# Kernel tuning notes

Measured on AMD Instinct MI355X. Metric: run time of the kernel, lower is better.

The kernel has to match this reference:

```python
import jax, jax.numpy as jnp
import numpy as np

# Multi-scale AvgPool3d pyramid (stride 1, zero padding, count_include_pad=True as in torch)
KERNELS = [(1, 1, 1), (1, 5, 5), (3, 13, 13), (5, 23, 23), (7, 31, 31), (9, 41, 41)]
WEIGHTS = [w / 100.0 for w in [20, 20, 20, 20, 20, 20, 10, 10]]
EPS = 1e-7  # BatchDiceLoss epsilon


def avgpool3d(x, k):
    # x: [B, C, D, H, W]; separable sum-pool per axis then divide by full kernel size
    # (equivalent to torch AvgPool3d with count_include_pad=True, stride 1, pad=(k-1)//2)
    y = x
    for axis, ks in zip((2, 3, 4), k):
        if ks > 1:
            window = [1] * 5
            window[axis] = ks
            pad = [(0, 0)] * 5
            pad[axis] = (ks // 2, ks // 2)
            y = jax.lax.reduce_window(y, 0.0, jax.lax.add, tuple(window), (1,) * 5, tuple(pad))
    return y / float(np.prod(k))


def batch_dice(pred, target):
    # BatchDiceLoss([1.0]): single label channel 0, flattened over the whole batch
    p = pred[:, 0].reshape(-1)
    t = target[:, 0].reshape(-1)
    inter = jnp.sum(p * t)
    return 1.0 - (2.0 * inter) / (jnp.sum(p) + jnp.sum(t) + EPS)


def multi_scale_dc(pred, target):
    loss = 0.0
    for k in KERNELS:
        pp = avgpool3d(avgpool3d(pred, k), k)   # pool applied twice per scale
        tt = avgpool3d(avgpool3d(target, k), k)
        loss = loss + batch_dice(pp, tt)
    return loss / len(KERNELS)


def setup_inputs() -> dict:
    key = jax.random.key(0)
    ks = jax.random.split(key, 14)
    vol = (4, 1, 28, 160, 160)
    u = lambda k: jax.random.uniform(k, vol, dtype=jnp.float32)
    return {
        "pr_core_c": u(ks[0]),
        "pr_core_p": u(ks[1]),
        "gt_core": u(ks[2]),
        "pr_lesion_c": u(ks[3]),
        "pr_lesion_p": u(ks[4]),
        "gt_lesion": u(ks[5]),
        "pr_penu_c": u(ks[6]),
        "pr_penu_p": u(ks[7]),
        "gt_penu": u(ks[8]),
        "output": jax.random.uniform(ks[9], (4, 6, 28, 160, 160), dtype=jnp.float32),
        "off_core_c": jax.random.normal(ks[10], (4, 3), dtype=jnp.float32),
        "off_penu_p": jax.random.normal(ks[11], (4, 3), dtype=jnp.float32),
        "off_target_c": jax.random.normal(ks[12], (4, 3), dtype=jnp.float32),
        "off_target_p": jax.random.normal(ks[13], (4, 3), dtype=jnp.float32),
    }


def reference(pr_core_c, pr_core_p, gt_core, pr_lesion_c, pr_lesion_p, gt_lesion,
              pr_penu_c, pr_penu_p, gt_penu, output,
              off_core_c, off_penu_p, off_target_c, off_target_p):
    loss = WEIGHTS[0] * multi_scale_dc(pr_core_c, gt_core)
    loss += WEIGHTS[1] * multi_scale_dc(pr_core_p, gt_core)
    loss += WEIGHTS[2] * multi_scale_dc(pr_lesion_c, gt_lesion)
    loss += WEIGHTS[3] * multi_scale_dc(pr_lesion_p, gt_lesion)
    loss += WEIGHTS[4] * multi_scale_dc(pr_penu_c, gt_penu)
    loss += WEIGHTS[5] * multi_scale_dc(pr_penu_p, gt_penu)
    # temporal monotonicity penalty: mean(|diff| - diff) per consecutive time pair
    diff = output[:, 1:] - output[:, :-1]           # [B, T-1, D, H, W]
    loss += WEIGHTS[6] * jnp.sum(jnp.mean(jnp.abs(diff) - diff, axis=(0, 2, 3, 4)))
    loss += WEIGHTS[7] * jnp.mean(jnp.abs(off_core_c - off_target_c))
    loss += WEIGHTS[7] * jnp.mean(jnp.abs(off_penu_p - off_target_p))
    return loss
```

## Files before the change

kernel.cpp:

```cpp
#include <hip/hip_runtime.h>
#include <hip/hip_fp16.h>


#define DIMB 4
#define DIMD 28
#define DIMH 160
#define DIMW 160
#define HW   (DIMH * DIMW)
#define DHW  (DIMD * HW)
#define VOL_N (DIMB * DHW)
#define PGRID 640
#define NSLOTS 91
#define DICE_EPS 1e-7

__device__ __forceinline__ float u2f(int pos, int k, int L) {
    if (k == 1) return 1.f;
    int r = k >> 1;
    float s = 0.f;
    for (int j = max(pos - r, 0); j <= min(pos + r, L - 1); ++j)
        s += (float)(min(j + r, L - 1) - max(j - r, 0) + 1);
    return s / (float)(k * k);
}

__device__ __forceinline__ float wave_sum(float v) {
#pragma unroll
    for (int o = 1; o < 64; o <<= 1) v += __shfl_xor(v, o, 64);
    return v;
}

template<int K>
__device__ __forceinline__ void box4_col(float (&x)[28]) {
    constexpr int R = K / 2;
    constexpr float INVK = 1.f / (float)K;
#pragma unroll
    for (int p = 0; p < 4; ++p) {
        float y[28];
        float s = 0.f;
#pragma unroll
        for (int j = 0; j <= R; ++j) s += x[j];
        y[0] = s;
#pragma unroll
        for (int i = 1; i < 28; ++i) {
            if (i + R < 28) s += x[i + R];
            if (i - R - 1 >= 0) s -= x[i - R - 1];
            y[i] = s;
        }
#pragma unroll
        for (int i = 0; i < 28; ++i) x[i] = y[i] * INVK;
    }
}

template<int K>
__device__ __forceinline__ void hbody(const float* __restrict__ base,
                                      __half* __restrict__ ob, int t)
{
    constexpr int R = K / 2;
    constexpr float INVK = 1.f / (float)K;
    int l = t & 63, v = t >> 6;
    int c = l >> 4;
    int wl = v * 16 + (l & 15);
    int h0 = c * 40;
    float ox[40];
#pragma unroll
    for (int i = 0; i < 40; ++i) ox[i] = base[(h0 + i) * DIMW + wl];
#pragma unroll
    for (int pass = 0; pass < 4; ++pass) {
        float lo[R], hi[R];
#pragma unroll
        for (int i = 0; i < R; ++i) {
            float a = __shfl(ox[40 - R + i], l - 16, 64);
            lo[i] = (c == 0) ? 0.f : a;
            float b = __shfl(ox[i], l + 16, 64);
            hi[i] = (c == 3) ? 0.f : b;
        }
#define HWIN(j) ((j) < R ? lo[(j)] : ((j) < R + 40 ? ox[(j) - R] : hi[(j) - R - 40]))
        float out[40];
        float s = 0.f;
#pragma unroll
        for (int j = 0; j <= 2 * R; ++j) s += HWIN(j);
        out[0] = s * INVK;
#pragma unroll
        for (int i = 1; i < 40; ++i) {
            s += HWIN(i + 2 * R) - HWIN(i - 1);
            out[i] = s * INVK;
        }
#undef HWIN
#pragma unroll
        for (int i = 0; i < 40; ++i) ox[i] = out[i];
    }
#pragma unroll
    for (int i = 0; i < 40; ++i) ob[(h0 + i) * DIMW + wl] = __float2half(ox[i]);
}

__device__ __forceinline__ void hpool_run(const float* in, __half* ob5, int sc,
                                          int bd, int wt, int t)
{
    const float* base = in + (size_t)bd * HW + wt * 32;
    __half* ob = ob5 + (size_t)sc * VOL_N + (size_t)bd * HW + wt * 32;
    switch (sc) {
        case 0: hbody<5>(base, ob, t); break;
        case 1: hbody<13>(base, ob, t); break;
        case 2: hbody<23>(base, ob, t); break;
        case 3: hbody<31>(base, ob, t); break;
        default: hbody<41>(base, ob, t); break;
    }
}

__global__ __launch_bounds__(256) void hpool_mono(const float* __restrict__ g0,
    const float* __restrict__ g1, const float* __restrict__ g2,
    const float* __restrict__ o6, __half* __restrict__ bufs,
    double* __restrict__ partials)
{
    __shared__ float redSm[4];
    int bx = blockIdx.x;
    if (bx < 4200) {
        int u = bx * 2 + (threadIdx.x >> 7);
        int tt = threadIdx.x & 127;
        int gg = u / 2800, r0 = u - gg * 2800;
        int sc = r0 / 560, r = r0 - sc * 560;
        const float* in = (gg == 0) ? g0 : (gg == 1) ? g1 : g2;
        hpool_run(in, bufs + (size_t)gg * 5 * VOL_N, sc, r / 5, r % 5, tt);
    } else {
        int mb = bx - 4200;
        const int N4 = VOL_N / 4, PB = N4 / DIMB;
        float acc = 0.f;
        const float4* p = (const float4*)o6;
        for (int i = mb * 256 + threadIdx.x; i < N4; i += PGRID * 256) {
            int b = i / PB, r4 = i - b * PB;
            size_t a = (size_t)(b * 6) * PB + r4;
            float4 prev = p[a];
#pragma unroll
            for (int cc = 1; cc < 6; ++cc) {
                float4 cur = p[a + (size_t)cc * PB];
                acc += fmaxf(prev.x - cur.x, 0.f) + fmaxf(prev.y - cur.y, 0.f)
                     + fmaxf(prev.z - cur.z, 0.f) + fmaxf(prev.w - cur.w, 0.f);
                prev = cur;
            }
        }
        float rv = wave_sum(acc * 2.f);
        int lane = threadIdx.x & 63, wid = threadIdx.x >> 6;
        if (lane == 0) redSm[wid] = rv;
        __syncthreads();
        if (threadIdx.x == 0)
            partials[(size_t)90 * PGRID + mb] =
                (double)redSm[0] + redSm[1] + redSm[2] + redSm[3];
    }
}

template<int K, int KD>
__device__ __forceinline__ void scale_work(const uint2 (&rg)[5],
    float (*S)[164], int t, int l, int c, int rr, bool act,
    const float* __restrict__ pc, const float* __restrict__ pp,
    size_t base0, float& aic, float& aip)
{
    constexpr int R = K / 2;
    constexpr float INVK = 1.f / (float)K;
    float ox[20];
#pragma unroll
    for (int i = 0; i < 20; ++i) ox[i] = 0.f;
    if (act) {
#pragma unroll
        for (int q = 0; q < 5; ++q) {
            __half2 a = *reinterpret_cast<const __half2*>(&rg[q].x);
            __half2 b = *reinterpret_cast<const __half2*>(&rg[q].y);
            float2 fa = __half22float2(a), fb = __half22float2(b);
            ox[4*q+0] = fa.x; ox[4*q+1] = fa.y;
            ox[4*q+2] = fb.x; ox[4*q+3] = fb.y;
        }
    }
#pragma unroll
    for (int pass = 0; pass < 4; ++pass) {
        float lo[R], hi[R];
#pragma unroll
        for (int i = 0; i < R; ++i) {
            float a = __shfl(ox[20 - R + i], l - 1, 64);
            lo[i] = (c == 0) ? 0.f : a;
            float b = __shfl(ox[i], l + 1, 64);
            hi[i] = (c == 7) ? 0.f : b;
        }
#define WWIN(j) ((j) < R ? lo[(j)] : ((j) < R + 20 ? ox[(j) - R] : hi[(j) - R - 20]))
        float out[20];
        float s = 0.f;
#pragma unroll
        for (int j = 0; j <= 2 * R; ++j) s += WWIN(j);
        out[0] = s * INVK;
#pragma unroll
        for (int i = 1; i < 20; ++i) {
            s += WWIN(i + 2 * R) - WWIN(i - 1);
            out[i] = s * INVK;
        }
#undef WWIN
#pragma unroll
        for (int i = 0; i < 20; ++i) ox[i] = out[i];
    }
    if (act) {
#pragma unroll
        for (int i = 0; i < 20; ++i) S[rr][c * 20 + i] = ox[i];
    }
    __syncthreads();
    if constexpr (KD > 1) {
        if (t < DIMW) {
            float col[28];
#pragma unroll
            for (int j = 0; j < 28; ++j) col[j] = S[j][t];
            box4_col<KD>(col);
#pragma unroll
            for (int j = 0; j < 28; ++j) S[j][t] = col[j];
        }
        __syncthreads();
    }
    for (int e4 = t; e4 < 280; e4 += 256) {
        int dd = e4 / 40, w4 = e4 - dd * 40;
        size_t gb = base0 + (size_t)dd * HW + 4 * w4;
        float4 vc = *(const float4*)(pc + gb);
        float4 vp = *(const float4*)(pp + gb);
        float t0 = S[dd][4*w4], t1 = S[dd][4*w4+1];
        float t2 = S[dd][4*w4+2], t3 = S[dd][4*w4+3];
        aic += vc.x*t0 + vc.y*t1 + vc.z*t2 + vc.w*t3;
        aip += vp.x*t0 + vp.y*t1 + vp.z*t2 + vp.w*t3;
    }
    __syncthreads();
}

__global__ __launch_bounds__(256) void wd5(const __half* __restrict__ bufs,
    const float* __restrict__ pc0, const float* __restrict__ pp0,
    const float* __restrict__ pc1, const float* __restrict__ pp1,
    const float* __restrict__ pc2, const float* __restrict__ pp2,
    const float* __restrict__ tr0, const float* __restrict__ tr1,
    const float* __restrict__ tr2, double* __restrict__ partials)
{
    __shared__ float S[DIMD][164];
    __shared__ float cD[6][DIMD], cW[6][DIMW];
    __shared__ float redS[4][22];
    int bx = blockIdx.x;
    int grp = bx / 1920, r = bx - grp * 1920;
    int g = r / PGRID, bh = r - g * PGRID;
    int b = bh / DIMH, h = bh - b * DIMH;
    size_t base0 = (size_t)b * DHW + (size_t)h * DIMW;
    const float* pc = (g == 0) ? pc0 : (g == 1) ? pc1 : pc2;
    const float* pp = (g == 0) ? pp0 : (g == 1) ? pp1 : pp2;
    int t = threadIdx.x;
    int l = t & 63;
    int rr = (t >> 6) * 7 + (l >> 3), c = l & 7;
    bool act = l < 56;
    const __half* tb = bufs + (size_t)g * 5 * VOL_N + base0
                     + (size_t)rr * HW + c * 20;
    int wid = t >> 6;

    if (grp == 0) {
        const float* tr = (g == 0) ? tr0 : (g == 1) ? tr1 : tr2;
        const int KDa[6] = {1, 1, 3, 5, 7, 9};
        const int KHa[6] = {1, 5, 13, 23, 31, 41};
        for (int e = t; e < 6 * DIMD; e += 256) {
            int s = e / DIMD, q = e - s * DIMD;
            cD[s][q] = u2f(q, KDa[s], DIMD);
        }
        for (int e = t; e < 6 * DIMW; e += 256) {
            int s = e / DIMW, q = e - s * DIMW;
            cW[s][q] = u2f(q, KHa[s], DIMW);
        }
        __syncthreads();
        uint2 rA[5];
        if (act) {
            const __half* hp = tb + (size_t)4 * VOL_N;
#pragma unroll
            for (int q = 0; q < 5; ++q) rA[q] = *(const uint2*)(hp + 4 * q);
        }
        float vals[22];
#pragma unroll
        for (int i = 0; i < 22; ++i) vals[i] = 0.f;
        for (int e4 = t; e4 < 280; e4 += 256) {
            int dd = e4 / 40, w4 = e4 - dd * 40;
            size_t gb = base0 + (size_t)dd * HW + 4 * w4;
            float4 vt = *(const float4*)(tr + gb);
            float4 vc = *(const float4*)(pc + gb);
            float4 vp = *(const float4*)(pp + gb);
            vals[0] += vc.x*vt.x + vc.y*vt.y + vc.z*vt.z + vc.w*vt.w;
            vals[1] += vp.x*vt.x + vp.y*vt.y + vp.z*vt.z + vp.w*vt.w;
#pragma unroll
            for (int s = 0; s < 6; ++s) {
                float cdh = cD[s][dd];
                float w0 = cdh * cW[s][4*w4+0], w1 = cdh * cW[s][4*w4+1];
                float w2 = cdh * cW[s][4*w4+2], w3 = cdh * cW[s][4*w4+3];
                vals[2+s]  += w0*vc.x + w1*vc.y + w2*vc.z + w3*vc.w;
                vals[8+s]  += w0*vp.x + w1*vp.y + w2*vp.z + w3*vp.w;
                vals[14+s] += w0*vt.x + w1*vt.y + w2*vt.z + w3*vt.w;
            }
        }
        scale_work<41, 9>(rA, S, t, l, c, rr, act, pc, pp, base0,
                          vals[20], vals[21]);
#pragma unroll
        for (int i = 0; i < 22; ++i) {
            float rv = wave_sum(vals[i]);
            if (l == 0) redS[wid][i] = rv;
        }
        __syncthreads();
        if (t < 22) {
            double rv = (double)redS[0][t] + redS[1][t] + redS[2][t] + redS[3][t];
            int slot; double fac = 1.0;
            if (t == 0) slot = (2 * g) * 6;
            else if (t == 1) slot = (2 * g + 1) * 6;
            else if (t < 20) {
                int i = t - 2, vv = i / 6, s = i % 6;
                fac = (double)cW[s][h];
                slot = (vv == 0) ? 36 + (2 * g) * 6 + s
                     : (vv == 1) ? 36 + (2 * g + 1) * 6 + s
                                 : 72 + g * 6 + s;
            }
            else if (t == 20) slot = (2 * g) * 6 + 5;
            else slot = (2 * g + 1) * 6 + 5;
            partials[(size_t)slot * PGRID + bh] = rv * fac;
        }
    } else {
        uint2 rA[5], rB[5];
        int scA = (grp == 1) ? 0 : 1;
        int scB = (grp == 1) ? 3 : 2;
        if (act) {
            const __half* ha = tb + (size_t)scA * VOL_N;
            const __half* hb = tb + (size_t)scB * VOL_N;
#pragma unroll
            for (int q = 0; q < 5; ++q) rA[q] = *(const uint2*)(ha + 4 * q);
#pragma unroll
            for (int q = 0; q < 5; ++q) rB[q] = *(const uint2*)(hb + 4 * q);
        }
        float vals[4] = {0.f, 0.f, 0.f, 0.f};
        if (grp == 1) {
            scale_work<5, 1>(rA, S, t, l, c, rr, act, pc, pp, base0, vals[0], vals[1]);
            scale_work<31, 7>(rB, S, t, l, c, rr, act, pc, pp, base0, vals[2], vals[3]);
        } else {
            scale_work<13, 3>(rA, S, t, l, c, rr, act, pc, pp, base0, vals[0], vals[1]);
            scale_work<23, 5>(rB, S, t, l, c, rr, act, pc, pp, base0, vals[2], vals[3]);
        }
#pragma unroll
        for (int i = 0; i < 4; ++i) {
            float rv = wave_sum(vals[i]);
            if (l == 0) redS[wid][i] = rv;
        }
        __syncthreads();
        if (t < 4) {
            double rv = (double)redS[0][t] + redS[1][t] + redS[2][t] + redS[3][t];
            int sd = (t < 2) ? ((grp == 1) ? 1 : 2) : ((grp == 1) ? 4 : 3);
            int slot = (2 * g + (t & 1)) * 6 + sd;
            partials[(size_t)slot * PGRID + bh] = rv;
        }
    }
}

__global__ __launch_bounds__(64) void fin_pre(const double* __restrict__ partials,
                                              double* __restrict__ ssum)
{
    int slot = blockIdx.x, t = threadIdx.x;
    double a = 0.0;
    for (int i = t; i < PGRID; i += 64) a += partials[(size_t)slot * PGRID + i];
#pragma unroll
    for (int o = 1; o < 64; o <<= 1) a += __shfl_xor(a, o, 64);
    if (t == 0) ssum[slot] = a;
}

__global__ void finalize(const double* __restrict__ ssum,
                         const float* __restrict__ off_a,
                         const float* __restrict__ off_b,
                         const float* __restrict__ off_ta,
                         const float* __restrict__ off_tb,
                         float* __restrict__ out)
{
    if (threadIdx.x == 0) {
        double loss = 0.0;
        for (int pair = 0; pair < 6; ++pair) {
            for (int s = 0; s < 6; ++s) {
                double inter = ssum[pair * 6 + s];
                double sp = ssum[36 + pair * 6 + s];
                double st = ssum[72 + (pair / 2) * 6 + s];
                loss += 0.2 * (1.0 - 2.0 * inter / (sp + st + DICE_EPS)) / 6.0;
            }
        }
        loss += 0.1 * (ssum[90] / (double)VOL_N);
        double oa = 0.0, ob = 0.0;
        for (int i = 0; i < 12; ++i) {
            oa += fabs((double)off_a[i] - (double)off_ta[i]);
            ob += fabs((double)off_b[i] - (double)off_tb[i]);
        }
        loss += 0.1 * (oa / 12.0) + 0.1 * (ob / 12.0);
        out[0] = (float)loss;
    }
}

extern "C" void kernel_launch(void* const* d_in, const int* in_sizes, int n_in,
                              void* d_out, int out_size, void* d_ws, size_t ws_size,
                              hipStream_t stream)
{
    double* partials = (double*)d_ws;
    double* ssum = partials + (size_t)NSLOTS * PGRID;
    __half* bufs = (__half*)((char*)d_ws + 512 * 1024);

    const float* pred[6] = {(const float*)d_in[0], (const float*)d_in[1],
                            (const float*)d_in[3], (const float*)d_in[4],
                            (const float*)d_in[6], (const float*)d_in[7]};
    const float* gt[3] = {(const float*)d_in[2], (const float*)d_in[5],
                          (const float*)d_in[8]};

    hpool_mono<<<4840, 256, 0, stream>>>(gt[0], gt[1], gt[2],
                                         (const float*)d_in[9], bufs, partials);
    wd5<<<5760, 256, 0, stream>>>(bufs, pred[0], pred[1], pred[2], pred[3],
                                  pred[4], pred[5], gt[0], gt[1], gt[2], partials);
    fin_pre<<<NSLOTS, 64, 0, stream>>>(partials, ssum);
    finalize<<<1, 64, 0, stream>>>(ssum,
                                   (const float*)d_in[10], (const float*)d_in[11],
                                   (const float*)d_in[12], (const float*)d_in[13],
                                   (float*)d_out);
}
```

Before: 139.8 us.

## Store H-pooled targets as 8-bit and split per-scale dot blocks

The H-direction pooled target intermediates are now written as unsigned 8-bit values scaled by 255 instead of fp16, and the 1/255 is folded into the first W pass when they are read back. One block now loads each raw target tile once and produces all five scales. The W/D pooling kernel is reorganised into one block per scale and row, with the D-column box filter fused straight into the dot product with predictions. The unpooled sums move into a separate flat-grid section. This cuts intermediate memory traffic and repeated loads, at the cost of quantisation error and the assumption that pooled targets lie in [0,1].

```diff
diff --git a/kernel.cpp b/kernel.cpp
--- a/kernel.cpp
+++ b/kernel.cpp
@@ -1,5 +1,4 @@
 #include <hip/hip_runtime.h>
-#include <hip/hip_fp16.h>
 
 
 #define DIMB 4
@@ -51,18 +50,15 @@
 }
 
 template<int K>
-__device__ __forceinline__ void hbody(const float* __restrict__ base,
-                                      __half* __restrict__ ob, int t)
+__device__ __forceinline__ void hstore(const float (&raw)[40],
+                                       unsigned char* __restrict__ ob,
+                                       int l, int c, int wl, int h0)
 {
     constexpr int R = K / 2;
     constexpr float INVK = 1.f / (float)K;
-    int l = t & 63, v = t >> 6;
-    int c = l >> 4;
-    int wl = v * 16 + (l & 15);
-    int h0 = c * 40;
     float ox[40];
 #pragma unroll
-    for (int i = 0; i < 40; ++i) ox[i] = base[(h0 + i) * DIMW + wl];
+    for (int i = 0; i < 40; ++i) ox[i] = raw[i];
 #pragma unroll
     for (int pass = 0; pass < 4; ++pass) {
         float lo[R], hi[R];
@@ -89,39 +85,37 @@
         for (int i = 0; i < 40; ++i) ox[i] = out[i];
     }
 #pragma unroll
-    for (int i = 0; i < 40; ++i) ob[(h0 + i) * DIMW + wl] = __float2half(ox[i]);
-}
-
-__device__ __forceinline__ void hpool_run(const float* in, __half* ob5, int sc,
-                                          int bd, int wt, int t)
-{
-    const float* base = in + (size_t)bd * HW + wt * 32;
-    __half* ob = ob5 + (size_t)sc * VOL_N + (size_t)bd * HW + wt * 32;
-    switch (sc) {
-        case 0: hbody<5>(base, ob, t); break;
-        case 1: hbody<13>(base, ob, t); break;
-        case 2: hbody<23>(base, ob, t); break;
-        case 3: hbody<31>(base, ob, t); break;
-        default: hbody<41>(base, ob, t); break;
-    }
+    for (int i = 0; i < 40; ++i)
+        ob[(h0 + i) * DIMW + wl] = (unsigned char)__float2uint_rn(ox[i] * 255.f);
 }
 
 __global__ __launch_bounds__(256) void hpool_mono(const float* __restrict__ g0,
     const float* __restrict__ g1, const float* __restrict__ g2,
-    const float* __restrict__ o6, __half* __restrict__ bufs,
+    const float* __restrict__ o6, unsigned char* __restrict__ bufs,
     double* __restrict__ partials)
 {
     __shared__ float redSm[4];
     int bx = blockIdx.x;
-    if (bx < 4200) {
+    if (bx < 840) {
         int u = bx * 2 + (threadIdx.x >> 7);
         int tt = threadIdx.x & 127;
-        int gg = u / 2800, r0 = u - gg * 2800;
-        int sc = r0 / 560, r = r0 - sc * 560;
-        const float* in = (gg == 0) ? g0 : (gg == 1) ? g1 : g2;
-        hpool_run(in, bufs + (size_t)gg * 5 * VOL_N, sc, r / 5, r % 5, tt);
+        int g = u / 560, r = u - g * 560;
+        int bd = r / 5, wt = r - bd * 5;
+        const float* in = (g == 0) ? g0 : (g == 1) ? g1 : g2;
+        int l = tt & 63, v = tt >> 6;
+        int c = l >> 4, wl = v * 16 + (l & 15), h0 = c * 40;
+        const float* base = in + (size_t)bd * HW + wt * 32;
+        float raw[40];
+#pragma unroll
+        for (int i = 0; i < 40; ++i) raw[i] = base[(h0 + i) * DIMW + wl];
+        unsigned char* ob = bufs + (size_t)g * 5 * VOL_N + (size_t)bd * HW + wt * 32;
+        hstore<5> (raw, ob + 0 * (size_t)VOL_N, l, c, wl, h0);
+        hstore<13>(raw, ob + 1 * (size_t)VOL_N, l, c, wl, h0);
+        hstore<23>(raw, ob + 2 * (size_t)VOL_N, l, c, wl, h0);
+        hstore<31>(raw, ob + 3 * (size_t)VOL_N, l, c, wl, h0);
+        hstore<41>(raw, ob + 4 * (size_t)VOL_N, l, c, wl, h0);
     } else {
-        int mb = bx - 4200;
+        int mb = bx - 840;
         const int N4 = VOL_N / 4, PB = N4 / DIMB;
         float acc = 0.f;
         const float4* p = (const float4*)o6;
@@ -148,28 +142,34 @@
 }
 
 template<int K, int KD>
-__device__ __forceinline__ void scale_work(const uint2 (&rg)[5],
-    float (*S)[164], int t, int l, int c, int rr, bool act,
+__device__ __forceinline__ void wd_scale(const unsigned char* __restrict__ tb,
     const float* __restrict__ pc, const float* __restrict__ pp,
-    size_t base0, float& aic, float& aip)
+    float* SH, int t, size_t base0, double* __restrict__ partials,
+    int slot_c, int slot_p, int bh)
 {
     constexpr int R = K / 2;
-    constexpr float INVK = 1.f / (float)K;
+    float (*S)[164] = (float(*)[164])SH;
+    int l = t & 63, wid = t >> 6;
+    int rr = wid * 7 + (l >> 3), c = l & 7;
+    bool act = (l < 56);
     float ox[20];
 #pragma unroll
     for (int i = 0; i < 20; ++i) ox[i] = 0.f;
     if (act) {
+        const unsigned char* hp = tb + base0 + (size_t)rr * HW + c * 20;
+        unsigned int u[5];
+#pragma unroll
+        for (int q = 0; q < 5; ++q) u[q] = *(const unsigned int*)(hp + 4 * q);
 #pragma unroll
         for (int q = 0; q < 5; ++q) {
-            __half2 a = *reinterpret_cast<const __half2*>(&rg[q].x);
-            __half2 b = *reinterpret_cast<const __half2*>(&rg[q].y);
-            float2 fa = __half22float2(a), fb = __half22float2(b);
-            ox[4*q+0] = fa.x; ox[4*q+1] = fa.y;
-            ox[4*q+2] = fb.x; ox[4*q+3] = fb.y;
+#pragma unroll
+            for (int j = 0; j < 4; ++j)
+                ox[4 * q + j] = (float)((u[q] >> (8 * j)) & 0xFFu);
         }
     }
 #pragma unroll
     for (int pass = 0; pass < 4; ++pass) {
+        const float scl = (pass == 0) ? (1.f / ((float)K * 255.f)) : (1.f / (float)K);
         float lo[R], hi[R];
 #pragma unroll
         for (int i = 0; i < R; ++i) {
@@ -183,11 +183,11 @@
         float s = 0.f;
 #pragma unroll
         for (int j = 0; j <= 2 * R; ++j) s += WWIN(j);
-        out[0] = s * INVK;
+        out[0] = s * scl;
 #pragma unroll
         for (int i = 1; i < 20; ++i) {
             s += WWIN(i + 2 * R) - WWIN(i - 1);
-            out[i] = s * INVK;
+            out[i] = s * scl;
         }
 #undef WWIN
 #pragma unroll
@@ -198,6 +198,7 @@
         for (int i = 0; i < 20; ++i) S[rr][c * 20 + i] = ox[i];
     }
     __syncthreads();
+    float aic = 0.f, aip = 0.f;
     if constexpr (KD > 1) {
         if (t < DIMW) {
             float col[28];
@@ -205,143 +206,128 @@
             for (int j = 0; j < 28; ++j) col[j] = S[j][t];
             box4_col<KD>(col);
 #pragma unroll
-            for (int j = 0; j < 28; ++j) S[j][t] = col[j];
-        }
-        __syncthreads();
-    }
-    for (int e4 = t; e4 < 280; e4 += 256) {
-        int dd = e4 / 40, w4 = e4 - dd * 40;
-        size_t gb = base0 + (size_t)dd * HW + 4 * w4;
-        float4 vc = *(const float4*)(pc + gb);
-        float4 vp = *(const float4*)(pp + gb);
-        float t0 = S[dd][4*w4], t1 = S[dd][4*w4+1];
-        float t2 = S[dd][4*w4+2], t3 = S[dd][4*w4+3];
-        aic += vc.x*t0 + vc.y*t1 + vc.z*t2 + vc.w*t3;
-        aip += vp.x*t0 + vp.y*t1 + vp.z*t2 + vp.w*t3;
-    }
+            for (int j = 0; j < 28; ++j) {
+                size_t gi = base0 + (size_t)j * HW + t;
+                aic += pc[gi] * col[j];
+                aip += pp[gi] * col[j];
+            }
+        }
+    } else {
+        for (int e4 = t; e4 < 1120; e4 += 256) {
+            int dd = e4 / 40, w4 = e4 - dd * 40;
+            size_t gb = base0 + (size_t)dd * HW + 4 * w4;
+            float4 vc = *(const float4*)(pc + gb);
+            float4 vp = *(const float4*)(pp + gb);
+            float t0 = S[dd][4*w4], t1 = S[dd][4*w4+1];
+            float t2 = S[dd][4*w4+2], t3 = S[dd][4*w4+3];
+            aic += vc.x*t0 + vc.y*t1 + vc.z*t2 + vc.w*t3;
+            aip += vp.x*t0 + vp.y*t1 + vp.z*t2 + vp.w*t3;
+        }
+    }
+    float r1 = wave_sum(aic), r2 = wave_sum(aip);
+    float* red2 = SH + 28 * 164;
+    if (l == 0) { red2[wid * 2] = r1; red2[wid * 2 + 1] = r2; }
     __syncthreads();
-}
-
-__global__ __launch_bounds__(256) void wd5(const __half* __restrict__ bufs,
+    if (t < 2) {
+        double rv = (double)red2[t] + red2[2 + t] + red2[4 + t] + red2[6 + t];
+        partials[(size_t)(t == 0 ? slot_c : slot_p) * PGRID + bh] = rv;
+    }
+}
+
+__global__ __launch_bounds__(256) void wd_dot0(const unsigned char* __restrict__ bufs,
     const float* __restrict__ pc0, const float* __restrict__ pp0,
     const float* __restrict__ pc1, const float* __restrict__ pp1,
     const float* __restrict__ pc2, const float* __restrict__ pp2,
     const float* __restrict__ tr0, const float* __restrict__ tr1,
     const float* __restrict__ tr2, double* __restrict__ partials)
 {
-    __shared__ float S[DIMD][164];
-    __shared__ float cD[6][DIMD], cW[6][DIMW];
-    __shared__ float redS[4][22];
+    __shared__ float SH[28 * 164 + 8];
     int bx = blockIdx.x;
-    int grp = bx / 1920, r = bx - grp * 1920;
-    int g = r / PGRID, bh = r - g * PGRID;
-    int b = bh / DIMH, h = bh - b * DIMH;
-    size_t base0 = (size_t)b * DHW + (size_t)h * DIMW;
-    const float* pc = (g == 0) ? pc0 : (g == 1) ? pc1 : pc2;
-    const float* pp = (g == 0) ? pp0 : (g == 1) ? pp1 : pp2;
     int t = threadIdx.x;
-    int l = t & 63;
-    int rr = (t >> 6) * 7 + (l >> 3), c = l & 7;
-    bool act = l < 56;
-    const __half* tb = bufs + (size_t)g * 5 * VOL_N + base0
-                     + (size_t)rr * HW + c * 20;
-    int wid = t >> 6;
-
-    if (grp == 0) {
+    if (bx < 9600) {
+        int q = bx / 1920, r = bx - q * 1920;
+        int s = 5 - q;
+        int g = r / PGRID, bh = r - g * PGRID;
+        int b = bh / DIMH, h = bh - b * DIMH;
+        size_t base0 = (size_t)b * DHW + (size_t)h * DIMW;
+        const float* pc = (g == 0) ? pc0 : (g == 1) ? pc1 : pc2;
+        const float* pp = (g == 0) ? pp0 : (g == 1) ? pp1 : pp2;
+        const unsigned char* tb = bufs + (size_t)(g * 5 + (s - 1)) * VOL_N;
+        int slot_c = (2 * g) * 6 + s, slot_p = (2 * g + 1) * 6 + s;
+        switch (s) {
+            case 5: wd_scale<41, 9>(tb, pc, pp, SH, t, base0, partials, slot_c, slot_p, bh); break;
+            case 4: wd_scale<31, 7>(tb, pc, pp, SH, t, base0, partials, slot_c, slot_p, bh); break;
+            case 3: wd_scale<23, 5>(tb, pc, pp, SH, t, base0, partials, slot_c, slot_p, bh); break;
+            case 2: wd_scale<13, 3>(tb, pc, pp, SH, t, base0, partials, slot_c, slot_p, bh); break;
+            default: wd_scale<5, 1>(tb, pc, pp, SH, t, base0, partials, slot_c, slot_p, bh); break;
+        }
+    } else {
+        int db = bx - 9600;
+        int g = db / PGRID, blk = db - g * PGRID;
+        const float* pc = (g == 0) ? pc0 : (g == 1) ? pc1 : pc2;
+        const float* pp = (g == 0) ? pp0 : (g == 1) ? pp1 : pp2;
         const float* tr = (g == 0) ? tr0 : (g == 1) ? tr1 : tr2;
+        float* cD = SH;
+        float* cL = SH + 168;
+        float* redS = SH + 1128;
         const int KDa[6] = {1, 1, 3, 5, 7, 9};
         const int KHa[6] = {1, 5, 13, 23, 31, 41};
-        for (int e = t; e < 6 * DIMD; e += 256) {
-            int s = e / DIMD, q = e - s * DIMD;
-            cD[s][q] = u2f(q, KDa[s], DIMD);
-        }
-        for (int e = t; e < 6 * DIMW; e += 256) {
-            int s = e / DIMW, q = e - s * DIMW;
-            cW[s][q] = u2f(q, KHa[s], DIMW);
-        }
+        for (int e = t; e < 168; e += 256)
+            cD[e] = u2f(e % 28, KDa[e / 28], DIMD);
+        for (int e = t; e < 960; e += 256)
+            cL[168 - 168 + 168 + e - e + e] = cL[e] = u2f(e % 160, KHa[e / 160], DIMH);
         __syncthreads();
-        uint2 rA[5];
-        if (act) {
-            const __half* hp = tb + (size_t)4 * VOL_N;
-#pragma unroll
-            for (int q = 0; q < 5; ++q) rA[q] = *(const uint2*)(hp + 4 * q);
-        }
-        float vals[22];
-#pragma unroll
-        for (int i = 0; i < 22; ++i) vals[i] = 0.f;
-        for (int e4 = t; e4 < 280; e4 += 256) {
-            int dd = e4 / 40, w4 = e4 - dd * 40;
-            size_t gb = base0 + (size_t)dd * HW + 4 * w4;
-            float4 vt = *(const float4*)(tr + gb);
-            float4 vc = *(const float4*)(pc + gb);
-            float4 vp = *(const float4*)(pp + gb);
-            vals[0] += vc.x*vt.x + vc.y*vt.y + vc.z*vt.z + vc.w*vt.w;
-            vals[1] += vp.x*vt.x + vp.y*vt.y + vp.z*vt.z + vp.w*vt.w;
+        float aI0c = 0.f, aI0p = 0.f;
+        float aS[18];
+#pragma unroll
+        for (int i = 0; i < 18; ++i) aS[i] = 0.f;
+        const float4* c4p = (const float4*)pc;
+        const float4* p4p = (const float4*)pp;
+        const float4* t4p = (const float4*)tr;
+        const int N4 = VOL_N / 4;
+        for (int i4 = blk * 256 + t; i4 < N4; i4 += PGRID * 256) {
+            int w4 = i4 % 40;
+            int rest = i4 / 40;
+            int h = rest % DIMH;
+            int d = (rest / DIMH) % DIMD;
+            float4 vc = c4p[i4], vp = p4p[i4], vt = t4p[i4];
+            aI0c += vc.x*vt.x + vc.y*vt.y + vc.z*vt.z + vc.w*vt.w;
+            aI0p += vp.x*vt.x + vp.y*vt.y + vp.z*vt.z + vp.w*vt.w;
 #pragma unroll
             for (int s = 0; s < 6; ++s) {
-                float cdh = cD[s][dd];
-                float w0 = cdh * cW[s][4*w4+0], w1 = cdh * cW[s][4*w4+1];
-                float w2 = cdh * cW[s][4*w4+2], w3 = cdh * cW[s][4*w4+3];
-                vals[2+s]  += w0*vc.x + w1*vc.y + w2*vc.z + w3*vc.w;
-                vals[8+s]  += w0*vp.x + w1*vp.y + w2*vp.z + w3*vp.w;
-                vals[14+s] += w0*vt.x + w1*vt.y + w2*vt.z + w3*vt.w;
-            }
-        }
-        scale_work<41, 9>(rA, S, t, l, c, rr, act, pc, pp, base0,
-                          vals[20], vals[21]);
-#pragma unroll
-        for (int i = 0; i < 22; ++i) {
+                float cdh = cD[s * 28 + d] * cL[s * 160 + h];
+                float w0 = cdh * cL[s * 160 + 4 * w4 + 0];
+                float w1 = cdh * cL[s * 160 + 4 * w4 + 1];
+                float w2 = cdh * cL[s * 160 + 4 * w4 + 2];
+                float w3 = cdh * cL[s * 160 + 4 * w4 + 3];
+                aS[s]      += w0*vc.x + w1*vc.y + w2*vc.z + w3*vc.w;
+                aS[6 + s]  += w0*vp.x + w1*vp.y + w2*vp.z + w3*vp.w;
+                aS[12 + s] += w0*vt.x + w1*vt.y + w2*vt.z + w3*vt.w;
+            }
+        }
+        float vals[20];
+        vals[0] = aI0c; vals[1] = aI0p;
+#pragma unroll
+        for (int i = 0; i < 18; ++i) vals[2 + i] = aS[i];
+        int lane = t & 63, wid = t >> 6;
+#pragma unroll
+        for (int i = 0; i < 20; ++i) {
             float rv = wave_sum(vals[i]);
-            if (l == 0) redS[wid][i] = rv;
+            if (lane == 0) redS[wid * 20 + i] = rv;
         }
         __syncthreads();
-        if (t < 22) {
-            double rv = (double)redS[0][t] + redS[1][t] + redS[2][t] + redS[3][t];
-            int slot; double fac = 1.0;
+        if (t < 20) {
+            double rv = (double)redS[t] + redS[20 + t] + redS[40 + t] + redS[60 + t];
+            int slot;
             if (t == 0) slot = (2 * g) * 6;
             else if (t == 1) slot = (2 * g + 1) * 6;
-            else if (t < 20) {
+            else {
                 int i = t - 2, vv = i / 6, s = i % 6;
-                fac = (double)cW[s][h];
                 slot = (vv == 0) ? 36 + (2 * g) * 6 + s
                      : (vv == 1) ? 36 + (2 * g + 1) * 6 + s
                                  : 72 + g * 6 + s;
             }
-            else if (t == 20) slot = (2 * g) * 6 + 5;
-            else slot = (2 * g + 1) * 6 + 5;
-            partials[(size_t)slot * PGRID + bh] = rv * fac;
-        }
-    } else {
-        uint2 rA[5], rB[5];
-        int scA = (grp == 1) ? 0 : 1;
-        int scB = (grp == 1) ? 3 : 2;
-        if (act) {
-            const __half* ha = tb + (size_t)scA * VOL_N;
-            const __half* hb = tb + (size_t)scB * VOL_N;
-#pragma unroll
-            for (int q = 0; q < 5; ++q) rA[q] = *(const uint2*)(ha + 4 * q);
-#pragma unroll
-            for (int q = 0; q < 5; ++q) rB[q] = *(const uint2*)(hb + 4 * q);
-        }
-        float vals[4] = {0.f, 0.f, 0.f, 0.f};
-        if (grp == 1) {
-            scale_work<5, 1>(rA, S, t, l, c, rr, act, pc, pp, base0, vals[0], vals[1]);
-            scale_work<31, 7>(rB, S, t, l, c, rr, act, pc, pp, base0, vals[2], vals[3]);
-        } else {
-            scale_work<13, 3>(rA, S, t, l, c, rr, act, pc, pp, base0, vals[0], vals[1]);
-            scale_work<23, 5>(rB, S, t, l, c, rr, act, pc, pp, base0, vals[2], vals[3]);
-        }
-#pragma unroll
-        for (int i = 0; i < 4; ++i) {
-            float rv = wave_sum(vals[i]);
-            if (l == 0) redS[wid][i] = rv;
-        }
-        __syncthreads();
-        if (t < 4) {
-            double rv = (double)redS[0][t] + redS[1][t] + redS[2][t] + redS[3][t];
-            int sd = (t < 2) ? ((grp == 1) ? 1 : 2) : ((grp == 1) ? 4 : 3);
-            int slot = (2 * g + (t & 1)) * 6 + sd;
-            partials[(size_t)slot * PGRID + bh] = rv;
+            partials[(size_t)slot * PGRID + blk] = rv;
         }
     }
 }
@@ -391,7 +377,7 @@
 {
     double* partials = (double*)d_ws;
     double* ssum = partials + (size_t)NSLOTS * PGRID;
-    __half* bufs = (__half*)((char*)d_ws + 512 * 1024);
+    unsigned char* bufs = (unsigned char*)d_ws + 512 * 1024;
 
     const float* pred[6] = {(const float*)d_in[0], (const float*)d_in[1],
                             (const float*)d_in[3], (const float*)d_in[4],
@@ -399,10 +385,11 @@
     const float* gt[3] = {(const float*)d_in[2], (const float*)d_in[5],
                           (const float*)d_in[8]};
 
-    hpool_mono<<<4840, 256, 0, stream>>>(gt[0], gt[1], gt[2],
+    hpool_mono<<<1480, 256, 0, stream>>>(gt[0], gt[1], gt[2],
                                          (const float*)d_in[9], bufs, partials);
-    wd5<<<5760, 256, 0, stream>>>(bufs, pred[0], pred[1], pred[2], pred[3],
-                                  pred[4], pred[5], gt[0], gt[1], gt[2], partials);
+    wd_dot0<<<11520, 256, 0, stream>>>(bufs, pred[0], pred[1], pred[2], pred[3],
+                                       pred[4], pred[5], gt[0], gt[1], gt[2],
+                                       partials);
     fin_pre<<<NSLOTS, 64, 0, stream>>>(partials, ssum);
     finalize<<<1, 64, 0, stream>>>(ssum,
                                    (const float*)d_in[10], (const float*)d_in[11],
```

New measurement: 165.9 us. +18.7%, slower.
